# Performance work log

Measured on AMD Instinct MI355X. Metric: run time of the kernel, lower is better.

## Reference

```python
import jax, jax.numpy as jnp
import numpy as np

B, N, F, H, L = 8, 512, 32, 64, 2

def setup_inputs() -> dict:
    key = jax.random.key(0)
    ks = jax.random.split(key, 16)
    s = lambda fan_in: 1.0 / np.sqrt(fan_in)
    return {
        "x": jax.random.normal(ks[0], (B, N, F), dtype=jnp.float32),
        # node encoder: Linear(F, H), stored as [in, out]
        "W_enc": jax.random.uniform(ks[1], (F, H), minval=-s(F), maxval=s(F)),
        "b_enc": jax.random.uniform(ks[2], (H,), minval=-s(F), maxval=s(F)),
        # edge MLP: Linear(2H, H) then Linear(H, 1)
        "W_e1": jax.random.uniform(ks[3], (2 * H, H), minval=-s(2 * H), maxval=s(2 * H)),
        "b_e1": jax.random.uniform(ks[4], (H,), minval=-s(2 * H), maxval=s(2 * H)),
        "W_e2": jax.random.uniform(ks[5], (H,), minval=-s(H), maxval=s(H)),
        "b_e2": jax.random.uniform(ks[6], (), minval=-s(H), maxval=s(H)),
        # per-layer message Linear(H, H)
        "W_msg": jax.random.uniform(ks[7], (L, H, H), minval=-s(H), maxval=s(H)),
        "b_msg": jax.random.uniform(ks[8], (L, H), minval=-s(H), maxval=s(H)),
        # per-layer GRUCell(H, H): gates ordered [r, z, n], stored as [in, 3H]
        "W_ih": jax.random.uniform(ks[9], (L, H, 3 * H), minval=-s(H), maxval=s(H)),
        "b_ih": jax.random.uniform(ks[10], (L, 3 * H), minval=-s(H), maxval=s(H)),
        "W_hh": jax.random.uniform(ks[11], (L, H, 3 * H), minval=-s(H), maxval=s(H)),
        "b_hh": jax.random.uniform(ks[12], (L, 3 * H), minval=-s(H), maxval=s(H)),
        # output Linear(H, 1)
        "W_out": jax.random.uniform(ks[13], (H, 1), minval=-s(H), maxval=s(H)),
        "b_out": jax.random.uniform(ks[14], (1,), minval=-s(H), maxval=s(H)),
    }

def reference(x, W_enc, b_enc, W_e1, b_e1, W_e2, b_e2, W_msg, b_msg,
              W_ih, b_ih, W_hh, b_hh, W_out, b_out):
    # Node encoding (dropout is eval-mode identity)
    h = jax.nn.relu(x @ W_enc + b_enc)  # [B, N, H]

    # Edge MLP on pairwise concat [h_i, h_j]: split W_e1 so we never build the 2H concat
    Wa, Wb = W_e1[:H], W_e1[H:]
    zi = h @ Wa                           # contribution of h_i, [B, N, H]
    zj = h @ Wb                           # contribution of h_j, [B, N, H]
    e = jax.nn.relu(zi[:, :, None, :] + zj[:, None, :, :] + b_e1)  # [B, N, N, H]
    logits = jnp.einsum('bijh,h->bij', e, W_e2) + b_e2             # [B, N, N]

    eye = jnp.eye(logits.shape[-1], dtype=bool)
    logits = jnp.where(eye[None], -jnp.inf, logits)
    adj = jax.nn.softmax(logits, axis=-1)
    adj = jnp.nan_to_num(adj, nan=0.0, posinf=0.0, neginf=0.0)

    for l in range(L):
        m = jnp.einsum('bij,bjh->bih', adj, h)             # message aggregation
        m = jax.nn.relu(m @ W_msg[l] + b_msg[l])
        # GRUCell update (gates [r, z, n])
        gi = m @ W_ih[l] + b_ih[l]
        gh = h @ W_hh[l] + b_hh[l]
        ir, iz, inn = jnp.split(gi, 3, axis=-1)
        hr, hz, hn = jnp.split(gh, 3, axis=-1)
        r = jax.nn.sigmoid(ir + hr)
        z = jax.nn.sigmoid(iz + hz)
        n = jnp.tanh(inn + r * hn)
        h = (1.0 - z) * n + z * h

    graph_emb = jnp.mean(h, axis=1)       # [B, H]
    return graph_emb @ W_out + b_out      # [B, 1]
```

## Files before the change

### kernel.cpp

```cpp
#include <hip/hip_runtime.h>
#include <math.h>

#define BB 8
#define NN 512
#define FF 32
#define HH 64
#define NEG_BIG (-1.0e30f)

__device__ __forceinline__ float lane_bcast(float v, int l) {
    return __int_as_float(__builtin_amdgcn_readlane(__float_as_int(v), l));
}

__global__ __launch_bounds__(256) void encode_kernel(
    const float* __restrict__ x, const float* __restrict__ W_enc,
    const float* __restrict__ b_enc, const float* __restrict__ W_e1,
    const float* __restrict__ b_e1,
    float* __restrict__ h, float* __restrict__ zi, float* __restrict__ zj)
{
    const int t = threadIdx.x;
    const int hh = t & 63;
    const int qu = __builtin_amdgcn_readfirstlane(t >> 6);
    const int gR = blockIdx.x * 4 + qu;

    const float* xrow = x + gR * FF;
    float acc = b_enc[hh];
#pragma unroll
    for (int k = 0; k < FF; ++k)
        acc = fmaf(xrow[k], W_enc[k * HH + hh], acc);
    const float hval = fmaxf(acc, 0.f);
    h[gR * HH + hh] = hval;

    float z1 = b_e1[hh], z2 = 0.f;
#pragma unroll 8
    for (int k = 0; k < HH; ++k) {
        const float hk = lane_bcast(hval, k);
        z1 = fmaf(hk, W_e1[k * HH + hh], z1);
        z2 = fmaf(hk, W_e1[(HH + k) * HH + hh], z2);
    }
    zi[gR * HH + hh] = z1;
    zj[gR * HH + hh] = z2;
}

__global__ __launch_bounds__(256) void adj_kernel(
    const float* __restrict__ zi, const float* __restrict__ zj,
    const float* __restrict__ W_e2, const float* __restrict__ b_e2,
    float* __restrict__ adj)
{
    const int b = blockIdx.x >> 7;
    const int i0 = (blockIdx.x & 127) << 2;
    const int t = threadIdx.x;
    const int qu = __builtin_amdgcn_readfirstlane(t >> 6);
    const int tj = t & 63;
    const int j0 = (qu << 7) + tj;
    const int j1 = j0 + 64;

    __shared__ float zjs[NN][17];
    __shared__ float red[4][8];

    const float be2 = b_e2[0];
    float acc0[4], acc1[4];
#pragma unroll
    for (int r = 0; r < 4; ++r) { acc0[r] = be2; acc1[r] = be2; }

    const float* zib = zi + (b * NN + i0) * HH;

    for (int kp = 0; kp < 4; ++kp) {
        __syncthreads();
        for (int idx = t; idx < NN * 16; idx += 256) {
            const int row = idx >> 4, c = idx & 15;
            zjs[row][c] = zj[(b * NN + row) * HH + (kp << 4) + c];
        }
        __syncthreads();
#pragma unroll
        for (int c = 0; c < 16; ++c) {
            const int k = (kp << 4) + c;
            const float w = W_e2[k];
            const float zj0 = zjs[j0][c];
            const float zj1 = zjs[j1][c];
#pragma unroll
            for (int r = 0; r < 4; ++r) {
                const float zv = zib[r * HH + k];
                acc0[r] = fmaf(fmaxf(zv + zj0, 0.f), w, acc0[r]);
                acc1[r] = fmaf(fmaxf(zv + zj1, 0.f), w, acc1[r]);
            }
        }
    }

#pragma unroll
    for (int r = 0; r < 4; ++r) {
        const int irow = i0 + r;
        if (j0 == irow) acc0[r] = NEG_BIG;
        if (j1 == irow) acc1[r] = NEG_BIG;
    }

    float wmax[4];
#pragma unroll
    for (int r = 0; r < 4; ++r) {
        float m = fmaxf(acc0[r], acc1[r]);
#pragma unroll
        for (int off = 32; off >= 1; off >>= 1) m = fmaxf(m, __shfl_xor(m, off));
        wmax[r] = m;
    }
    if (tj == 0) {
#pragma unroll
        for (int r = 0; r < 4; ++r) red[qu][r] = wmax[r];
    }
    __syncthreads();
    float M[4];
#pragma unroll
    for (int r = 0; r < 4; ++r)
        M[r] = fmaxf(fmaxf(red[0][r], red[1][r]), fmaxf(red[2][r], red[3][r]));
    __syncthreads();

    float e0[4], e1[4];
#pragma unroll
    for (int r = 0; r < 4; ++r) {
        e0[r] = __expf(acc0[r] - M[r]);
        e1[r] = __expf(acc1[r] - M[r]);
        float s = e0[r] + e1[r];
#pragma unroll
        for (int off = 32; off >= 1; off >>= 1) s += __shfl_xor(s, off);
        if (tj == 0) red[qu][r] = s;
    }
    __syncthreads();
#pragma unroll
    for (int r = 0; r < 4; ++r) {
        const float inv = 1.0f / (red[0][r] + red[1][r] + red[2][r] + red[3][r]);
        float* arow = adj + ((size_t)(b * NN + i0 + r)) * NN;
        arow[j0] = e0[r] * inv;
        arow[j1] = e1[r] * inv;
    }
}

__global__ __launch_bounds__(1024) void layer_kernel(
    const float* __restrict__ adjw, const float* __restrict__ h_in,
    const float* __restrict__ Wmsg, const float* __restrict__ bmsg,
    const float* __restrict__ Wih, const float* __restrict__ bih,
    const float* __restrict__ Whh, const float* __restrict__ bhh,
    float* __restrict__ h_out)
{
    const int b  = blockIdx.x >> 5;
    const int i0 = (blockIdx.x & 31) << 4;
    const int t  = threadIdx.x;
    const int hh = t & 63;
    const int w  = __builtin_amdgcn_readfirstlane(t >> 6);
    const int gR0 = b * NN + i0;

    __shared__ union {
        float red[8][16][66];
        float gbuf[2][16][3][66];
    } U;
    __shared__ float mfull[16][66];
    __shared__ float mmfull[16][66];
    __shared__ float hown[16][66];

    hown[w][hh] = h_in[(size_t)(gR0 + w) * HH + hh];

    const int rg = w >> 3, kc = w & 7;
    const float* hb = h_in + (size_t)b * NN * HH;
    const float* arow = adjw + (size_t)(gR0 + rg * 8) * NN + kc * 64;
    const float* hj = hb + (size_t)(kc * 64) * HH + hh;

    float mac[8] = {0.f, 0.f, 0.f, 0.f, 0.f, 0.f, 0.f, 0.f};
#pragma unroll 2
    for (int j = 0; j < 64; j += 4) {
        const float h0 = hj[(j + 0) * HH];
        const float h1 = hj[(j + 1) * HH];
        const float h2 = hj[(j + 2) * HH];
        const float h3 = hj[(j + 3) * HH];
#pragma unroll
        for (int r = 0; r < 8; ++r) {
            const float* ar = arow + (size_t)r * NN + j;
            mac[r] = fmaf(ar[3], h3,
                     fmaf(ar[2], h2,
                     fmaf(ar[1], h1,
                     fmaf(ar[0], h0, mac[r]))));
        }
    }
#pragma unroll
    for (int r = 0; r < 8; ++r) U.red[kc][rg * 8 + r][hh] = mac[r];
    __syncthreads();

    {
        float s = 0.f;
#pragma unroll
        for (int p = 0; p < 8; ++p) s += U.red[p][w][hh];
        mfull[w][hh] = s;

        float acc = bmsg[hh];
#pragma unroll 4
        for (int k = 0; k < HH; ++k)
            acc = fmaf(mfull[w][k], Wmsg[k * HH + hh], acc);
        mmfull[w][hh] = fmaxf(acc, 0.f);
    }
    __syncthreads();

    const int half = w >> 3, rp = w & 7;
    {
        const float* Wg = half ? Whh : Wih;
        const float* bg = half ? bhh : bih;
        const float (*src)[66] = half ? (const float (*)[66])hown
                                      : (const float (*)[66])mmfull;
        float a0 = bg[hh], a1 = bg[64 + hh], a2 = bg[128 + hh];
        float c0 = a0, c1 = a1, c2 = a2;
#pragma unroll 4
        for (int k = 0; k < HH; ++k) {
            const float* wk = Wg + k * 192;
            const float w0 = wk[hh], w1 = wk[64 + hh], w2 = wk[128 + hh];
            const float va = src[2 * rp][k];
            const float vb = src[2 * rp + 1][k];
            a0 = fmaf(va, w0, a0); a1 = fmaf(va, w1, a1); a2 = fmaf(va, w2, a2);
            c0 = fmaf(vb, w0, c0); c1 = fmaf(vb, w1, c1); c2 = fmaf(vb, w2, c2);
        }
        U.gbuf[half][2 * rp][0][hh] = a0;
        U.gbuf[half][2 * rp][1][hh] = a1;
        U.gbuf[half][2 * rp][2][hh] = a2;
        U.gbuf[half][2 * rp + 1][0][hh] = c0;
        U.gbuf[half][2 * rp + 1][1][hh] = c1;
        U.gbuf[half][2 * rp + 1][2][hh] = c2;
    }
    __syncthreads();

    {
        const float ir = U.gbuf[0][w][0][hh], iz = U.gbuf[0][w][1][hh],
                    in = U.gbuf[0][w][2][hh];
        const float hr = U.gbuf[1][w][0][hh], hz = U.gbuf[1][w][1][hh],
                    hn = U.gbuf[1][w][2][hh];
        const float rr = 1.f / (1.f + __expf(-(ir + hr)));
        const float zz = 1.f / (1.f + __expf(-(iz + hz)));
        const float nnv = tanhf(in + rr * hn);
        h_out[(size_t)(gR0 + w) * HH + hh] = (1.f - zz) * nnv + zz * hown[w][hh];
    }
}

__global__ __launch_bounds__(1024) void readout_kernel(
    const float* __restrict__ h, const float* __restrict__ W_out,
    const float* __restrict__ b_out, float* __restrict__ out)
{
    const int b = blockIdx.x;
    const int t = threadIdx.x;
    const int hh = t & 63;
    const int w = t >> 6;
    __shared__ float red[16][65];

    float s = 0.f;
#pragma unroll 4
    for (int i = w; i < NN; i += 16) s += h[((size_t)(b * NN + i)) * HH + hh];
    red[w][hh] = s;
    __syncthreads();
    if (w == 0) {
        float tot = 0.f;
#pragma unroll
        for (int r = 0; r < 16; ++r) tot += red[r][hh];
        float v = tot * (1.0f / NN) * W_out[hh];
#pragma unroll
        for (int off = 32; off >= 1; off >>= 1) v += __shfl_xor(v, off);
        if (hh == 0) out[b] = v + b_out[0];
    }
}

extern "C" void kernel_launch(void* const* d_in, const int* in_sizes, int n_in,
                              void* d_out, int out_size, void* d_ws, size_t ws_size,
                              hipStream_t stream)
{
    const float* x     = (const float*)d_in[0];
    const float* W_enc = (const float*)d_in[1];
    const float* b_enc = (const float*)d_in[2];
    const float* W_e1  = (const float*)d_in[3];
    const float* b_e1  = (const float*)d_in[4];
    const float* W_e2  = (const float*)d_in[5];
    const float* b_e2  = (const float*)d_in[6];
    const float* W_msg = (const float*)d_in[7];
    const float* b_msg = (const float*)d_in[8];
    const float* W_ih  = (const float*)d_in[9];
    const float* b_ih  = (const float*)d_in[10];
    const float* W_hh  = (const float*)d_in[11];
    const float* b_hh  = (const float*)d_in[12];
    const float* W_out = (const float*)d_in[13];
    const float* b_out = (const float*)d_in[14];
    float* out = (float*)d_out;

    float* ws  = (float*)d_ws;
    float* h0  = ws;
    float* h1  = h0 + BB * NN * HH;
    float* zi  = h1 + BB * NN * HH;
    float* zj  = zi + BB * NN * HH;
    float* adjw = zj + BB * NN * HH;

    encode_kernel<<<BB * NN / 4, 256, 0, stream>>>(x, W_enc, b_enc, W_e1, b_e1, h0, zi, zj);
    adj_kernel<<<BB * (NN / 4), 256, 0, stream>>>(zi, zj, W_e2, b_e2, adjw);

    layer_kernel<<<BB * (NN / 16), 1024, 0, stream>>>(
        adjw, h0, W_msg, b_msg, W_ih, b_ih, W_hh, b_hh, h1);
    layer_kernel<<<BB * (NN / 16), 1024, 0, stream>>>(
        adjw, h1, W_msg + HH * HH, b_msg + HH,
        W_ih + HH * 3 * HH, b_ih + 3 * HH, W_hh + HH * 3 * HH, b_hh + 3 * HH, h0);

    readout_kernel<<<BB, 1024, 0, stream>>>(h0, W_out, b_out, out);
}
```

Measured before the change: 82.77 us.

## Stage adjacency in LDS, broadcast zi and x via readlane, fuse readout partials

The adjacency kernel now keeps its zi rows and W_e2 in registers and broadcasts them with readlane, and it fills the zj tile with float4 loads. The encoder also broadcasts x with readlane. The layer kernel copies its 16x512 adjacency tile into LDS with vectorized loads and reads it back as float4. The last layer writes per-block column sums, so readout only reduces 32 partials per graph instead of rereading h. The added 32KB of LDS per 1024-thread block may limit occupancy, and the __syncthreads inside the divergent-free final section depends on the partial pointer being uniform.

After: 83.19 us. Within noise of the previous version (+0.5%).

```diff
diff --git a/kernel.cpp b/kernel.cpp
--- a/kernel.cpp
+++ b/kernel.cpp
@@ -22,11 +22,11 @@
     const int qu = __builtin_amdgcn_readfirstlane(t >> 6);
     const int gR = blockIdx.x * 4 + qu;
 
-    const float* xrow = x + gR * FF;
+    const float xv = x[gR * FF + (hh & 31)];
     float acc = b_enc[hh];
-#pragma unroll
+#pragma unroll 8
     for (int k = 0; k < FF; ++k)
-        acc = fmaf(xrow[k], W_enc[k * HH + hh], acc);
+        acc = fmaf(lane_bcast(xv, k), W_enc[k * HH + hh], acc);
     const float hval = fmaxf(acc, 0.f);
     h[gR * HH + hh] = hval;
 
@@ -57,29 +57,38 @@
     __shared__ float zjs[NN][17];
     __shared__ float red[4][8];
 
+    float zr[4];
+#pragma unroll
+    for (int r = 0; r < 4; ++r) zr[r] = zi[(b * NN + i0 + r) * HH + tj];
+    const float wv = W_e2[tj];
+
     const float be2 = b_e2[0];
     float acc0[4], acc1[4];
 #pragma unroll
     for (int r = 0; r < 4; ++r) { acc0[r] = be2; acc1[r] = be2; }
 
-    const float* zib = zi + (b * NN + i0) * HH;
-
     for (int kp = 0; kp < 4; ++kp) {
         __syncthreads();
-        for (int idx = t; idx < NN * 16; idx += 256) {
-            const int row = idx >> 4, c = idx & 15;
-            zjs[row][c] = zj[(b * NN + row) * HH + (kp << 4) + c];
+        {
+            const int idx4 = t;
+#pragma unroll
+            for (int u = 0; u < 8; ++u) {
+                const int i4 = idx4 + u * 256;
+                const int row = i4 >> 2, c4 = i4 & 3;
+                *(float4*)&zjs[row][c4 * 4] =
+                    ((const float4*)(zj + (size_t)(b * NN + row) * HH))[kp * 4 + c4];
+            }
         }
         __syncthreads();
 #pragma unroll
         for (int c = 0; c < 16; ++c) {
             const int k = (kp << 4) + c;
-            const float w = W_e2[k];
+            const float w = lane_bcast(wv, k);
             const float zj0 = zjs[j0][c];
             const float zj1 = zjs[j1][c];
 #pragma unroll
             for (int r = 0; r < 4; ++r) {
-                const float zv = zib[r * HH + k];
+                const float zv = lane_bcast(zr[r], k);
                 acc0[r] = fmaf(fmaxf(zv + zj0, 0.f), w, acc0[r]);
                 acc1[r] = fmaf(fmaxf(zv + zj1, 0.f), w, acc1[r]);
             }
@@ -132,12 +141,12 @@
     }
 }
 
-__global__ __launch_bounds__(1024) void layer_kernel(
+__global__ __launch_bounds__(1024, 4) void layer_kernel(
     const float* __restrict__ adjw, const float* __restrict__ h_in,
     const float* __restrict__ Wmsg, const float* __restrict__ bmsg,
     const float* __restrict__ Wih, const float* __restrict__ bih,
     const float* __restrict__ Whh, const float* __restrict__ bhh,
-    float* __restrict__ h_out)
+    float* __restrict__ h_out, float* __restrict__ partial)
 {
     const int b  = blockIdx.x >> 5;
     const int i0 = (blockIdx.x & 31) << 4;
@@ -146,6 +155,7 @@
     const int w  = __builtin_amdgcn_readfirstlane(t >> 6);
     const int gR0 = b * NN + i0;
 
+    __shared__ float adjs[16][512];
     __shared__ union {
         float red[8][16][66];
         float gbuf[2][16][3][66];
@@ -154,12 +164,17 @@
     __shared__ float mmfull[16][66];
     __shared__ float hown[16][66];
 
+    {
+        const float4* asrc = (const float4*)(adjw + (size_t)gR0 * NN);
+        float4* adst = (float4*)&adjs[0][0];
+        adst[t] = asrc[t];
+        adst[t + 1024] = asrc[t + 1024];
+    }
     hown[w][hh] = h_in[(size_t)(gR0 + w) * HH + hh];
+    __syncthreads();
 
     const int rg = w >> 3, kc = w & 7;
-    const float* hb = h_in + (size_t)b * NN * HH;
-    const float* arow = adjw + (size_t)(gR0 + rg * 8) * NN + kc * 64;
-    const float* hj = hb + (size_t)(kc * 64) * HH + hh;
+    const float* hj = h_in + (size_t)b * NN * HH + (size_t)(kc * 64) * HH + hh;
 
     float mac[8] = {0.f, 0.f, 0.f, 0.f, 0.f, 0.f, 0.f, 0.f};
 #pragma unroll 2
@@ -170,11 +185,11 @@
         const float h3 = hj[(j + 3) * HH];
 #pragma unroll
         for (int r = 0; r < 8; ++r) {
-            const float* ar = arow + (size_t)r * NN + j;
-            mac[r] = fmaf(ar[3], h3,
-                     fmaf(ar[2], h2,
-                     fmaf(ar[1], h1,
-                     fmaf(ar[0], h0, mac[r]))));
+            const float4 av = *(const float4*)&adjs[rg * 8 + r][kc * 64 + j];
+            mac[r] = fmaf(av.w, h3,
+                     fmaf(av.z, h2,
+                     fmaf(av.y, h1,
+                     fmaf(av.x, h0, mac[r]))));
         }
     }
 #pragma unroll
@@ -188,7 +203,7 @@
         mfull[w][hh] = s;
 
         float acc = bmsg[hh];
-#pragma unroll 4
+#pragma unroll 8
         for (int k = 0; k < HH; ++k)
             acc = fmaf(mfull[w][k], Wmsg[k * HH + hh], acc);
         mmfull[w][hh] = fmaxf(acc, 0.f);
@@ -203,7 +218,7 @@
                                       : (const float (*)[66])mmfull;
         float a0 = bg[hh], a1 = bg[64 + hh], a2 = bg[128 + hh];
         float c0 = a0, c1 = a1, c2 = a2;
-#pragma unroll 4
+#pragma unroll 2
         for (int k = 0; k < HH; ++k) {
             const float* wk = Wg + k * 192;
             const float w0 = wk[hh], w1 = wk[64 + hh], w2 = wk[128 + hh];
@@ -229,34 +244,36 @@
         const float rr = 1.f / (1.f + __expf(-(ir + hr)));
         const float zz = 1.f / (1.f + __expf(-(iz + hz)));
         const float nnv = tanhf(in + rr * hn);
-        h_out[(size_t)(gR0 + w) * HH + hh] = (1.f - zz) * nnv + zz * hown[w][hh];
-    }
-}
-
-__global__ __launch_bounds__(1024) void readout_kernel(
-    const float* __restrict__ h, const float* __restrict__ W_out,
+        const float hnew = (1.f - zz) * nnv + zz * hown[w][hh];
+        h_out[(size_t)(gR0 + w) * HH + hh] = hnew;
+
+        if (partial != nullptr) {
+            mfull[w][hh] = hnew;
+            __syncthreads();
+            if (w == 0) {
+                float s = 0.f;
+#pragma unroll
+                for (int r = 0; r < 16; ++r) s += mfull[r][hh];
+                partial[blockIdx.x * 64 + hh] = s;
+            }
+        }
+    }
+}
+
+__global__ __launch_bounds__(64) void readout_kernel(
+    const float* __restrict__ partial, const float* __restrict__ W_out,
     const float* __restrict__ b_out, float* __restrict__ out)
 {
     const int b = blockIdx.x;
-    const int t = threadIdx.x;
-    const int hh = t & 63;
-    const int w = t >> 6;
-    __shared__ float red[16][65];
-
+    const int hh = threadIdx.x;
     float s = 0.f;
-#pragma unroll 4
-    for (int i = w; i < NN; i += 16) s += h[((size_t)(b * NN + i)) * HH + hh];
-    red[w][hh] = s;
-    __syncthreads();
-    if (w == 0) {
-        float tot = 0.f;
-#pragma unroll
-        for (int r = 0; r < 16; ++r) tot += red[r][hh];
-        float v = tot * (1.0f / NN) * W_out[hh];
-#pragma unroll
-        for (int off = 32; off >= 1; off >>= 1) v += __shfl_xor(v, off);
-        if (hh == 0) out[b] = v + b_out[0];
-    }
+#pragma unroll 8
+    for (int c = 0; c < 32; ++c)
+        s += partial[(b * 32 + c) * 64 + hh];
+    float v = s * (1.0f / NN) * W_out[hh];
+#pragma unroll
+    for (int off = 32; off >= 1; off >>= 1) v += __shfl_xor(v, off);
+    if (hh == 0) out[b] = v + b_out[0];
 }
 
 extern "C" void kernel_launch(void* const* d_in, const int* in_sizes, int n_in,
@@ -285,16 +302,18 @@
     float* h1  = h0 + BB * NN * HH;
     float* zi  = h1 + BB * NN * HH;
     float* zj  = zi + BB * NN * HH;
-    float* adjw = zj + BB * NN * HH;
+    float* prt = zj + BB * NN * HH;
+    float* adjw = prt + 256 * 64;
 
     encode_kernel<<<BB * NN / 4, 256, 0, stream>>>(x, W_enc, b_enc, W_e1, b_e1, h0, zi, zj);
     adj_kernel<<<BB * (NN / 4), 256, 0, stream>>>(zi, zj, W_e2, b_e2, adjw);
 
     layer_kernel<<<BB * (NN / 16), 1024, 0, stream>>>(
-        adjw, h0, W_msg, b_msg, W_ih, b_ih, W_hh, b_hh, h1);
+        adjw, h0, W_msg, b_msg, W_ih, b_ih, W_hh, b_hh, h1, nullptr);
     layer_kernel<<<BB * (NN / 16), 1024, 0, stream>>>(
         adjw, h1, W_msg + HH * HH, b_msg + HH,
-        W_ih + HH * 3 * HH, b_ih + 3 * HH, W_hh + HH * 3 * HH, b_hh + 3 * HH, h0);
-
-    readout_kernel<<<BB, 1024, 0, stream>>>(h0, W_out, b_out, out);
-}
+        W_ih + HH * 3 * HH, b_ih + 3 * HH, W_hh + HH * 3 * HH, b_hh + 3 * HH,
+        h0, prt);
+
+    readout_kernel<<<BB, 64, 0, stream>>>(prt, W_out, b_out, out);
+}
```
